# Kernel tuning notes

Hardware: AMD Instinct MI355X
Metric: run time of the kernel (lower is better)

## Reference

```python
import jax, jax.numpy as jnp
import numpy as np

N, D, H, E = 32768, 1024, 1024, 4


def setup_inputs() -> dict:
    key = jax.random.key(0)
    ks = jax.random.split(key, 10)
    s = 0.02  # xavier-ish init scale for stability
    return {
        "features": jax.random.normal(ks[0], (N, D), dtype=jnp.float32),
        "symbol_ids": jax.random.randint(ks[1], (N,), 0, E, dtype=jnp.int32),
        "W1": jax.random.normal(ks[2], (E, D, H), dtype=jnp.float32) * s,
        "b1": jax.random.normal(ks[3], (E, H), dtype=jnp.float32) * s,
        "W2": jax.random.normal(ks[4], (E, H, H), dtype=jnp.float32) * s,
        "b2": jax.random.normal(ks[5], (E, H), dtype=jnp.float32) * s,
        "W3": jax.random.normal(ks[6], (E, H, 1), dtype=jnp.float32) * s,
        "b3": jax.random.normal(ks[7], (E, 1), dtype=jnp.float32) * s,
        "slope": jax.random.normal(ks[8], (E,), dtype=jnp.float32),
        "intercept": jax.random.normal(ks[9], (E,), dtype=jnp.float32),
    }


def reference(features, symbol_ids, W1, b1, W2, b2, W3, b3, slope, intercept):
    # Run every atom through every expert MLP (E is tiny), then select by symbol.
    # h1: [E, N, H]
    h = jax.nn.relu(jnp.einsum("nd,edh->enh", features, W1) + b1[:, None, :])
    h = jax.nn.relu(jnp.einsum("enh,ehk->enk", h, W2) + b2[:, None, :])
    y = (jnp.einsum("enk,eko->eno", h, W3) + b3[:, None, :])[..., 0]  # [E, N]
    per_atom = slope[:, None] * y + intercept[:, None]                # [E, N]
    sel = symbol_ids[None, :] == jnp.arange(E, dtype=symbol_ids.dtype)[:, None]
    atomic_energies = jnp.sum(jnp.where(sel, per_atom, 0.0), axis=0)  # [N]
    image_energy = jnp.sum(atomic_energies)                           # scalar
    return image_energy
```

## Files before the change

### kernel.cpp

```cpp
#include <hip/hip_runtime.h>
#include <hip/hip_bf16.h>
#include <stdint.h>

#define NATOMS 32768
#define DDIM   1024
#define HDIM   1024
#define ENUM   4
#define MCAP   33792
#define MT256  132

typedef unsigned short u16;
typedef unsigned char  u8;
typedef __attribute__((ext_vector_type(8)))  int   i32x8;
typedef __attribute__((ext_vector_type(16))) float f32x16;

static const size_t XP_OFF   = 0;
static const size_t H1_OFF   = XP_OFF  + (size_t)MCAP * 1024;
static const size_t W1T_OFF  = H1_OFF  + (size_t)MCAP * 1024;
static const size_t W2T_OFF  = W1T_OFF + (size_t)ENUM * 1024 * 1024;
static const size_t PERM_OFF = W2T_OFF + (size_t)ENUM * 1024 * 1024;
static const size_t META_OFF = PERM_OFF + (size_t)MCAP * 4;

__device__ __forceinline__ u8 f2fp8(float x) {
    int w = __builtin_amdgcn_cvt_pk_fp8_f32(x, x, 0, false);
    return (u8)(w & 0xFF);
}

__global__ void k_count(const int* __restrict__ sym, int* __restrict__ meta) {
    __shared__ int cnt[4];
    int t = threadIdx.x;
    if (t < 4) cnt[t] = 0;
    __syncthreads();
    int n = blockIdx.x * 256 + t;
    int lane = t & 63;
    int e = sym[n];
#pragma unroll
    for (int j = 0; j < ENUM; ++j) {
        unsigned long long mask = __ballot(e == j);
        if (mask) {
            int leader = __ffsll((long long)mask) - 1;
            if (lane == leader) atomicAdd(&cnt[j], __popcll(mask));
        }
    }
    __syncthreads();
    if (t < 4) meta[256 + blockIdx.x * 4 + t] = cnt[t];
}

__global__ void k_offsets(int* __restrict__ meta, const float* __restrict__ slope,
                          const float* __restrict__ b3, const float* __restrict__ inter,
                          float* __restrict__ out) {
    __shared__ int tot[4];
    int t = threadIdx.x;
    if (t < 4) {
        int s = 0;
#pragma unroll 8
        for (int b = 0; b < 128; ++b) s += meta[256 + b * 4 + t];
        tot[t] = s;
    }
    __syncthreads();
    if (t == 0) {
        int off = 0;
        float c = 0.f;
        for (int e = 0; e < 4; ++e) {
            int cnt = tot[e];
            meta[e * 16]     = cnt;
            meta[128 + e]    = off;
            meta[64 + e*16]  = off;
            c += (float)cnt * (slope[e] * b3[e] + inter[e]);
            off += (cnt + 255) & ~255;
        }
        meta[132] = off;
        out[0] = c;
    }
}

__global__ void k_scatter(const int* __restrict__ sym, int* __restrict__ meta,
                          int* __restrict__ perm) {
    int n = blockIdx.x * 256 + threadIdx.x;
    int lane = threadIdx.x & 63;
    int e = sym[n];
#pragma unroll
    for (int j = 0; j < ENUM; ++j) {
        unsigned long long mask = __ballot(e == j);
        if (mask) {
            int leader = __ffsll((long long)mask) - 1;
            int base = 0;
            if (lane == leader)
                base = atomicAdd(&meta[64 + j * 16], __popcll(mask));
            base = __shfl(base, leader, 64);
            if (e == j) {
                int rank = __popcll(mask & ((1ull << lane) - 1ull));
                perm[base + rank] = n;
            }
        }
    }
}

__global__ void k_convx(const float* __restrict__ F, const int* __restrict__ perm,
                        const int* __restrict__ meta, u8* __restrict__ Xp) {
    int g = blockIdx.x * 256 + threadIdx.x;
    int slot = g >> 7, c = g & 127;
    const int* offs = meta + 128;
    int e = (slot >= offs[1]) + (slot >= offs[2]) + (slot >= offs[3]);
    bool valid = slot < offs[e] + meta[e * 16];
    uint2 v;
    if (!valid) {
        v.x = 0u; v.y = 0u;
    } else {
        int src = perm[slot];
        const float* fp = F + (size_t)src * 1024 + c * 8;
        int w0 = 0, w1 = 0;
        w0 = __builtin_amdgcn_cvt_pk_fp8_f32(fp[0], fp[1], w0, false);
        w0 = __builtin_amdgcn_cvt_pk_fp8_f32(fp[2], fp[3], w0, true);
        w1 = __builtin_amdgcn_cvt_pk_fp8_f32(fp[4], fp[5], w1, false);
        w1 = __builtin_amdgcn_cvt_pk_fp8_f32(fp[6], fp[7], w1, true);
        v.x = (unsigned)w0; v.y = (unsigned)w1;
    }
    *(uint2*)(void*)(Xp + (size_t)g * 8) = v;
}

__global__ void k_transw(const float* __restrict__ W1, u8* __restrict__ W1T,
                         const float* __restrict__ W2, u8* __restrict__ W2T) {
    __shared__ u8 tile[64][65];
    const float* W  = blockIdx.z ? W2  : W1;
    u8*          WT = blockIdx.z ? W2T : W1T;
    int e  = blockIdx.y;
    int tn = blockIdx.x & 15;
    int tk = blockIdx.x >> 4;
    const float* Wp = W  + (size_t)e * 1024 * 1024;
    u8*         WTp = WT + (size_t)e * 1024 * 1024;
    int c = threadIdx.x & 63, r0 = threadIdx.x >> 6;
#pragma unroll
    for (int i = 0; i < 16; ++i) {
        int r = r0 + i * 4;
        tile[r][c] = f2fp8(32.0f * Wp[(size_t)(tk * 64 + r) * 1024 + tn * 64 + c]);
    }
    __syncthreads();
#pragma unroll
    for (int i = 0; i < 16; ++i) {
        int r = r0 + i * 4;
        WTp[(size_t)(tn * 64 + r) * 1024 + tk * 64 + c] = tile[c][r];
    }
}

template <bool FUSE>
__global__ __launch_bounds__(512, 2)
void k_gemm(const u8* __restrict__ A, const u8* __restrict__ BT,
            const float* __restrict__ bias, u8* __restrict__ C,
            const int* __restrict__ meta, const float* __restrict__ W3,
            const float* __restrict__ slope, float* __restrict__ out) {
    __shared__ u8 As[2][32768];
    __shared__ u8 Bs[2][32768];
    const int* offs = meta + 128;

    const int flat = blockIdx.y * 8 + blockIdx.x;
    const int wgid = (flat & 7) * 66 + (flat >> 3);
    const int mt = wgid >> 2;
    const int nt = wgid & 3;
    const int m0 = mt * 256, n0 = nt * 256;
    if (m0 >= meta[132]) return;
    const int e = (m0 >= offs[1]) + (m0 >= offs[2]) + (m0 >= offs[3]);

    const int t = threadIdx.x;
    const int w = t >> 6, lane = t & 63;
    const int l31 = lane & 31, khalf = lane >> 5;
    const int wm = w & 1, wn = w >> 1;

    const u8* Ag = A  + (size_t)m0 * 1024;
    const u8* Bg = BT + (size_t)e * 1024 * 1024 + (size_t)n0 * 1024;

    const int srow = t >> 3;
    const int gcol = ((t & 7) ^ (srow & 7)) * 16;

    f32x16 acc[4][2] = {};

#define STAGE(buf, kt)                                                          \
    do {                                                                        \
        const size_t kb = (size_t)(kt) * 128;                                   \
        _Pragma("unroll")                                                       \
        for (int i = 0; i < 4; ++i) {                                           \
            __builtin_amdgcn_global_load_lds(                                   \
                (const void*)(Ag + (size_t)(i * 64 + srow) * 1024 + kb + gcol), \
                (void*)(&As[buf][i * 8192 + w * 1024]), 16, 0, 0);              \
            __builtin_amdgcn_global_load_lds(                                   \
                (const void*)(Bg + (size_t)(i * 64 + srow) * 1024 + kb + gcol), \
                (void*)(&Bs[buf][i * 8192 + w * 1024]), 16, 0, 0);              \
        }                                                                       \
    } while (0)

    STAGE(0, 0);

#pragma unroll 2
    for (int kt = 0; kt < 8; ++kt) {
        const int cur = kt & 1;
        asm volatile("" ::: "memory");
        __builtin_amdgcn_s_barrier();
        asm volatile("" ::: "memory");
        if (kt < 7) {
            STAGE(cur ^ 1, kt + 1);
            asm volatile("s_waitcnt vmcnt(8)" ::: "memory");
        } else {
            asm volatile("s_waitcnt vmcnt(0)" ::: "memory");
        }
        __builtin_amdgcn_s_barrier();
        asm volatile("" ::: "memory");

        const u8* Ab = &As[cur][0];
        const u8* Bb = &Bs[cur][0];

        i32x8 b[2][2];
#pragma unroll
        for (int ni = 0; ni < 2; ++ni)
#pragma unroll
            for (int ks = 0; ks < 2; ++ks) {
                int n = wn * 64 + ni * 32 + l31;
                int c0 = 4 * ks + 2 * khalf;
                const u8* base = Bb + n * 128;
                int lo = ((c0 ^ (n & 7)) << 4);
                union { uint4 q[2]; i32x8 v; } u;
                u.q[0] = *(const uint4*)(const void*)(base + lo);
                u.q[1] = *(const uint4*)(const void*)(base + (lo ^ 16));
                b[ni][ks] = u.v;
            }

#pragma unroll
        for (int mi = 0; mi < 4; ++mi) {
            i32x8 a[2];
#pragma unroll
            for (int ks = 0; ks < 2; ++ks) {
                int m = wm * 128 + mi * 32 + l31;
                int c0 = 4 * ks + 2 * khalf;
                const u8* base = Ab + m * 128;
                int lo = ((c0 ^ (m & 7)) << 4);
                union { uint4 q[2]; i32x8 v; } u;
                u.q[0] = *(const uint4*)(const void*)(base + lo);
                u.q[1] = *(const uint4*)(const void*)(base + (lo ^ 16));
                a[ks] = u.v;
            }
            __builtin_amdgcn_s_setprio(1);
#pragma unroll
            for (int ni = 0; ni < 2; ++ni)
#pragma unroll
                for (int ks = 0; ks < 2; ++ks)
                    acc[mi][ni] = __builtin_amdgcn_mfma_scale_f32_32x32x64_f8f6f4(
                        a[ks], b[ni][ks], acc[mi][ni],
                        0, 0,
                        0, 0x7F7F7F7F,
                        0, 0x7A7A7A7A);
            __builtin_amdgcn_s_setprio(0);
        }
    }
#undef STAGE

    if (!FUSE) {
#pragma unroll
        for (int ni = 0; ni < 2; ++ni) {
            int col = n0 + wn * 64 + ni * 32 + l31;
            float bv = bias[e * 1024 + col];
#pragma unroll
            for (int mi = 0; mi < 4; ++mi) {
                int rowb = m0 + wm * 128 + mi * 32 + 4 * khalf;
#pragma unroll
                for (int reg = 0; reg < 16; ++reg) {
                    int rowg = rowb + (reg & 3) + 8 * (reg >> 2);
                    float v = acc[mi][ni][reg] + bv;
                    v = v > 0.f ? v : 0.f;
                    C[(size_t)rowg * 1024 + col] = f2fp8(v);
                }
            }
        }
    } else {
        const int segEnd = offs[e] + meta[e * 16];
        const float se = slope[e];
        float psum = 0.f;
#pragma unroll
        for (int ni = 0; ni < 2; ++ni) {
            int col = n0 + wn * 64 + ni * 32 + l31;
            float bv  = bias[e * 1024 + col];
            float w3s = W3[e * 1024 + col] * se;
#pragma unroll
            for (int mi = 0; mi < 4; ++mi) {
                int rowb = m0 + wm * 128 + mi * 32 + 4 * khalf;
#pragma unroll
                for (int reg = 0; reg < 16; ++reg) {
                    int rowg = rowb + (reg & 3) + 8 * (reg >> 2);
                    float v = acc[mi][ni][reg] + bv;
                    v = v > 0.f ? v : 0.f;
                    psum += (rowg < segEnd) ? v * w3s : 0.f;
                }
            }
        }
#pragma unroll
        for (int o = 32; o; o >>= 1) psum += __shfl_xor(psum, o, 64);
        __syncthreads();
        float* red = (float*)As;
        if (lane == 0) red[w] = psum;
        __syncthreads();
        if (t == 0) {
            float s = 0.f;
#pragma unroll
            for (int i = 0; i < 8; ++i) s += red[i];
            atomicAdd(out, s);
        }
    }
}

extern "C" void kernel_launch(void* const* d_in, const int* in_sizes, int n_in,
                              void* d_out, int out_size, void* d_ws, size_t ws_size,
                              hipStream_t stream) {
    const float* features = (const float*)d_in[0];
    const int*   sym      = (const int*)d_in[1];
    const float* W1       = (const float*)d_in[2];
    const float* b1       = (const float*)d_in[3];
    const float* W2       = (const float*)d_in[4];
    const float* b2       = (const float*)d_in[5];
    const float* W3       = (const float*)d_in[6];
    const float* b3       = (const float*)d_in[7];
    const float* slope    = (const float*)d_in[8];
    const float* inter    = (const float*)d_in[9];
    float* out = (float*)d_out;

    char* ws  = (char*)d_ws;
    u8*  Xp   = (u8*)(ws + XP_OFF);
    u8*  H1b  = (u8*)(ws + H1_OFF);
    u8*  W1T  = (u8*)(ws + W1T_OFF);
    u8*  W2T  = (u8*)(ws + W2T_OFF);
    int* perm = (int*)(ws + PERM_OFF);
    int* meta = (int*)(ws + META_OFF);

    k_count<<<NATOMS / 256, 256, 0, stream>>>(sym, meta);
    k_offsets<<<1, 256, 0, stream>>>(meta, slope, b3, inter, out);
    k_scatter<<<NATOMS / 256, 256, 0, stream>>>(sym, meta, perm);
    k_convx<<<(MCAP * 128) / 256, 256, 0, stream>>>(features, perm, meta, Xp);
    k_transw<<<dim3(256, 4, 2), 256, 0, stream>>>(W1, W1T, W2, W2T);
    k_gemm<false><<<dim3(8, 66), 512, 0, stream>>>(Xp, W1T, b1, H1b, meta,
                                                   nullptr, nullptr, nullptr);
    k_gemm<true><<<dim3(8, 66), 512, 0, stream>>>(H1b, W2T, b2, nullptr, meta,
                                                  W3, slope, out);
}
```

Measured before the change: 377.3 us.

## Interleave next-tile LDS staging with MFMA sub-blocks using finer barriers

The single bulk prefetch of the next K tile is split into four row-chunk pairs. One pair is issued before the wait, and the other three are interleaved between the per-mi fragment loads and their MFMA groups. Barriers now separate each sub-step, so global-to-LDS traffic is spread across the compute phase instead of bursting at the start of each iteration. The cost is several extra workgroup barriers per K iteration and a tighter vmcnt wait whose correctness depends on the order in which loads are issued.

```diff
diff --git a/kernel.cpp b/kernel.cpp
--- a/kernel.cpp
+++ b/kernel.cpp
@@ -174,39 +174,60 @@
 
     f32x16 acc[4][2] = {};
 
-#define STAGE(buf, kt)                                                          \
+#define SPAIR(buf, ktile, i)                                                    \
     do {                                                                        \
-        const size_t kb = (size_t)(kt) * 128;                                   \
+        const size_t kb = (size_t)(ktile) * 128;                                \
+        __builtin_amdgcn_global_load_lds(                                       \
+            (const void*)(Ag + (size_t)((i) * 64 + srow) * 1024 + kb + gcol),   \
+            (void*)(&As[buf][(i) * 8192 + w * 1024]), 16, 0, 0);                \
+        __builtin_amdgcn_global_load_lds(                                       \
+            (const void*)(Bg + (size_t)((i) * 64 + srow) * 1024 + kb + gcol),   \
+            (void*)(&Bs[buf][(i) * 8192 + w * 1024]), 16, 0, 0);                \
+    } while (0)
+
+#define FRAG(dst, basep, rowsel, c0)                                            \
+    do {                                                                        \
+        int lo_ = (((c0) ^ ((rowsel) & 7)) << 4);                               \
+        union { uint4 q[2]; i32x8 v; } u_;                                      \
+        u_.q[0] = *(const uint4*)(const void*)((basep) + lo_);                  \
+        u_.q[1] = *(const uint4*)(const void*)((basep) + (lo_ ^ 16));           \
+        dst = u_.v;                                                             \
+    } while (0)
+
+#define MFMA4(mi, av)                                                           \
+    do {                                                                        \
+        __builtin_amdgcn_s_setprio(1);                                          \
         _Pragma("unroll")                                                       \
-        for (int i = 0; i < 4; ++i) {                                           \
-            __builtin_amdgcn_global_load_lds(                                   \
-                (const void*)(Ag + (size_t)(i * 64 + srow) * 1024 + kb + gcol), \
-                (void*)(&As[buf][i * 8192 + w * 1024]), 16, 0, 0);              \
-            __builtin_amdgcn_global_load_lds(                                   \
-                (const void*)(Bg + (size_t)(i * 64 + srow) * 1024 + kb + gcol), \
-                (void*)(&Bs[buf][i * 8192 + w * 1024]), 16, 0, 0);              \
-        }                                                                       \
+        for (int ni_ = 0; ni_ < 2; ++ni_)                                       \
+            _Pragma("unroll")                                                   \
+            for (int ks_ = 0; ks_ < 2; ++ks_)                                   \
+                acc[mi][ni_] = __builtin_amdgcn_mfma_scale_f32_32x32x64_f8f6f4( \
+                    (av)[ks_], b[ni_][ks_], acc[mi][ni_],                       \
+                    0, 0,                                 \
+                    0, 0x7F7F7F7F,                         \
+                    0, 0x7A7A7A7A);                        \
+        __builtin_amdgcn_s_setprio(0);                                          \
     } while (0)
 
-    STAGE(0, 0);
+#define FENCE asm volatile("" ::: "memory")
+#define BAR   do { FENCE; __builtin_amdgcn_s_barrier(); FENCE; } while (0)
+
+#pragma unroll
+    for (int i = 0; i < 4; ++i) SPAIR(0, 0, i);
 
 #pragma unroll 2
     for (int kt = 0; kt < 8; ++kt) {
         const int cur = kt & 1;
-        asm volatile("" ::: "memory");
-        __builtin_amdgcn_s_barrier();
-        asm volatile("" ::: "memory");
+        const u8* Ab = &As[cur][0];
+        const u8* Bb = &Bs[cur][0];
+
         if (kt < 7) {
-            STAGE(cur ^ 1, kt + 1);
-            asm volatile("s_waitcnt vmcnt(8)" ::: "memory");
+            SPAIR(cur ^ 1, kt + 1, 0);
+            asm volatile("s_waitcnt vmcnt(2)" ::: "memory");
         } else {
             asm volatile("s_waitcnt vmcnt(0)" ::: "memory");
         }
-        __builtin_amdgcn_s_barrier();
-        asm volatile("" ::: "memory");
-
-        const u8* Ab = &As[cur][0];
-        const u8* Bb = &Bs[cur][0];
+        BAR;
 
         i32x8 b[2][2];
 #pragma unroll
@@ -214,43 +235,36 @@
 #pragma unroll
             for (int ks = 0; ks < 2; ++ks) {
                 int n = wn * 64 + ni * 32 + l31;
-                int c0 = 4 * ks + 2 * khalf;
-                const u8* base = Bb + n * 128;
-                int lo = ((c0 ^ (n & 7)) << 4);
-                union { uint4 q[2]; i32x8 v; } u;
-                u.q[0] = *(const uint4*)(const void*)(base + lo);
-                u.q[1] = *(const uint4*)(const void*)(base + (lo ^ 16));
-                b[ni][ks] = u.v;
+                FRAG(b[ni][ks], Bb + n * 128, n, 4 * ks + 2 * khalf);
             }
-
-#pragma unroll
-        for (int mi = 0; mi < 4; ++mi) {
-            i32x8 a[2];
-#pragma unroll
-            for (int ks = 0; ks < 2; ++ks) {
-                int m = wm * 128 + mi * 32 + l31;
-                int c0 = 4 * ks + 2 * khalf;
-                const u8* base = Ab + m * 128;
-                int lo = ((c0 ^ (m & 7)) << 4);
-                union { uint4 q[2]; i32x8 v; } u;
-                u.q[0] = *(const uint4*)(const void*)(base + lo);
-                u.q[1] = *(const uint4*)(const void*)(base + (lo ^ 16));
-                a[ks] = u.v;
-            }
-            __builtin_amdgcn_s_setprio(1);
-#pragma unroll
-            for (int ni = 0; ni < 2; ++ni)
-#pragma unroll
-                for (int ks = 0; ks < 2; ++ks)
-                    acc[mi][ni] = __builtin_amdgcn_mfma_scale_f32_32x32x64_f8f6f4(
-                        a[ks], b[ni][ks], acc[mi][ni],
-                        0, 0,
-                        0, 0x7F7F7F7F,
-                        0, 0x7A7A7A7A);
-            __builtin_amdgcn_s_setprio(0);
-        }
-    }
-#undef STAGE
+        {
+            i32x8 a0[2];
+            int m = wm * 128 + 0 * 32 + l31;
+#pragma unroll
+            for (int ks = 0; ks < 2; ++ks)
+                FRAG(a0[ks], Ab + m * 128, m, 4 * ks + 2 * khalf);
+            MFMA4(0, a0);
+        }
+        BAR;
+
+#pragma unroll
+        for (int mi = 1; mi < 4; ++mi) {
+            i32x8 am[2];
+            int m = wm * 128 + mi * 32 + l31;
+#pragma unroll
+            for (int ks = 0; ks < 2; ++ks)
+                FRAG(am[ks], Ab + m * 128, m, 4 * ks + 2 * khalf);
+            if (kt < 7) SPAIR(cur ^ 1, kt + 1, mi);
+            BAR;
+            MFMA4(mi, am);
+            BAR;
+        }
+    }
+#undef SPAIR
+#undef FRAG
+#undef MFMA4
+#undef FENCE
+#undef BAR
 
     if (!FUSE) {
 #pragma unroll
```

Measured after the change: 724.0 us. +91.9%, slower.
